# Optimization experiments

Hardware: AMD Instinct MI355X
Metric: run time of the kernel (lower is better)

Reference implementation:

```python
import jax, jax.numpy as jnp
import numpy as np

NUM_HEADS = 12
LN_EPS = 1e-5


def _pe(seq_len, d_model):
    # sinusoidal positional encoding buffer (constant)
    pos = np.arange(seq_len, dtype=np.float32)[:, None]
    div = np.exp(np.arange(0, d_model, 2, dtype=np.float32) * (-np.log(10000.0) / d_model))
    pe = np.zeros((seq_len, d_model), dtype=np.float32)
    pe[:, 0::2] = np.sin(pos * div)
    pe[:, 1::2] = np.cos(pos * div)
    return jnp.asarray(pe)


def _ln(x, g, b):
    m = jnp.mean(x, axis=-1, keepdims=True)
    v = jnp.mean(jnp.square(x - m), axis=-1, keepdims=True)
    return (x - m) * jax.lax.rsqrt(v + LN_EPS) * g + b


def setup_inputs() -> dict:
    key = jax.random.key(0)
    B, S, V, D, L, F = 8, 512, 32000, 768, 4, 3072
    ks = jax.random.split(key, 8)
    sc = 0.02
    return {
        "x_ids": jax.random.randint(ks[0], (B, S), 0, V),
        "emb": jax.random.normal(ks[1], (V, D), jnp.float32) * sc,
        "Wq": jax.random.normal(ks[2], (L, D, D), jnp.float32) * sc,
        "bq": jnp.zeros((L, D), jnp.float32),
        "Wk": jax.random.normal(ks[3], (L, D, D), jnp.float32) * sc,
        "bk": jnp.zeros((L, D), jnp.float32),
        "Wv": jax.random.normal(ks[4], (L, D, D), jnp.float32) * sc,
        "bv": jnp.zeros((L, D), jnp.float32),
        "Wo": jax.random.normal(ks[5], (L, D, D), jnp.float32) * sc,
        "bo": jnp.zeros((L, D), jnp.float32),
        "g1": jnp.ones((L, D), jnp.float32),
        "bn1": jnp.zeros((L, D), jnp.float32),
        "W1": jax.random.normal(ks[6], (L, D, F), jnp.float32) * sc,
        "bw1": jnp.zeros((L, F), jnp.float32),
        "W2": jax.random.normal(ks[7], (L, F, D), jnp.float32) * sc,
        "bw2": jnp.zeros((L, D), jnp.float32),
        "g2": jnp.ones((L, D), jnp.float32),
        "bn2": jnp.zeros((L, D), jnp.float32),
    }


def reference(x_ids, emb, Wq, bq, Wk, bk, Wv, bv, Wo, bo, g1, bn1, W1, bw1, W2, bw2, g2, bn2):
    B, S = x_ids.shape
    D = emb.shape[1]
    H = NUM_HEADS
    dk = D // H
    h = emb[x_ids] + _pe(S, D)  # [B,S,D]; dropout is identity (eval)

    def layer(h, p):
        wq, bq_, wk, bk_, wv, bv_, wo, bo_, g1_, bn1_, w1, b1_, w2, b2_, g2_, bn2_ = p

        def heads(y):  # [B,S,D] -> [B,H,S,dk]
            return y.reshape(B, S, H, dk).transpose(0, 2, 1, 3)

        q = heads(h @ wq + bq_)
        k = heads(h @ wk + bk_)
        v = heads(h @ wv + bv_)
        scores = jnp.einsum('bhqd,bhkd->bhqk', q, k) / jnp.sqrt(jnp.float32(dk))
        attn = jax.nn.softmax(scores, axis=-1)
        o = jnp.einsum('bhqk,bhkd->bhqd', attn, v)
        o = o.transpose(0, 2, 1, 3).reshape(B, S, D)
        h = _ln(h + o @ wo + bo_, g1_, bn1_)
        ff = jax.nn.relu(h @ w1 + b1_) @ w2 + b2_
        h = _ln(h + ff, g2_, bn2_)
        return h, None

    h, _ = jax.lax.scan(layer, h, (Wq, bq, Wk, bk, Wv, bv, Wo, bo, g1, bn1, W1, bw1, W2, bw2, g2, bn2))
    return h
```

## Files before the change

### kernel.cpp

```cpp
#include <hip/hip_runtime.h>
#include <stdint.h>

#define B_ 8
#define S_ 512
#define D_ 768
#define H_ 12
#define DK_ 64
#define F_ 3072
#define L_ 4
#define NT_ (B_*S_)
#define BH_ (B_*H_)
#define DQKV_ 2304

typedef __bf16 bf16x8 __attribute__((ext_vector_type(8)));
typedef float f32x4 __attribute__((ext_vector_type(4)));

static __device__ __forceinline__ unsigned short f2b(float f){
  union { float f; unsigned u; } x; x.f = f;
  unsigned r = x.u + 0x7fffu + ((x.u >> 16) & 1u);
  return (unsigned short)(r >> 16);
}
static __device__ __forceinline__ float b2f(unsigned short u){
  union { unsigned u; float f; } x; x.u = ((unsigned)u) << 16; return x.f;
}

static __device__ __forceinline__ void gload16(const void* g, void* l){
  __builtin_amdgcn_global_load_lds((const __attribute__((address_space(1))) void*)g,
                                   (__attribute__((address_space(3))) void*)l, 16, 0, 0);
}

static __device__ __forceinline__ float wsum(float v){
  #pragma unroll
  for (int off = 32; off; off >>= 1) v += __shfl_xor(v, off);
  return v;
}

__global__ void wconv_kernel(const float* __restrict__ in, unsigned short* __restrict__ out,
                             int R, int C, size_t outLS, int rowBase){
  __shared__ float tile[64][33];
  const int l = blockIdx.z;
  in  += (size_t)l*R*C;
  out += (size_t)l*outLS;
  const int c0 = blockIdx.x*32, r0 = blockIdx.y*64;
  const int tx = threadIdx.x, ty = threadIdx.y;
  #pragma unroll
  for (int i = 0; i < 8; ++i)
    tile[ty+8*i][tx] = in[(size_t)(r0+ty+8*i)*C + c0+tx];
  __syncthreads();
  #pragma unroll
  for (int p = 0; p < 4; ++p) {
    const int c = p*8 + ty;
    ushort2 u;
    u.x = f2b(tile[tx*2][c]);
    u.y = f2b(tile[tx*2+1][c]);
    *reinterpret_cast<ushort2*>(&out[(size_t)(rowBase + c0 + c)*R + r0 + tx*2]) = u;
  }
}

__global__ void wconvqkv_kernel(const float* __restrict__ Wq, const float* __restrict__ Wk,
                                const float* __restrict__ Wv, unsigned short* __restrict__ out){
  __shared__ float tile[64][33];
  const int z = blockIdx.z;
  const int l = z / 3, which = z % 3;
  const float* in = (which == 0 ? Wq : which == 1 ? Wk : Wv) + (size_t)l*D_*D_;
  unsigned short* o = out + (size_t)l*DQKV_*D_;
  const int rowBase = which*D_;
  const int c0 = blockIdx.x*32, r0 = blockIdx.y*64;
  const int tx = threadIdx.x, ty = threadIdx.y;
  #pragma unroll
  for (int i = 0; i < 8; ++i)
    tile[ty+8*i][tx] = in[(size_t)(r0+ty+8*i)*D_ + c0+tx];
  __syncthreads();
  #pragma unroll
  for (int p = 0; p < 4; ++p) {
    const int c = p*8 + ty;
    ushort2 u;
    u.x = f2b(tile[tx*2][c]);
    u.y = f2b(tile[tx*2+1][c]);
    *reinterpret_cast<ushort2*>(&o[(size_t)(rowBase + c0 + c)*D_ + r0 + tx*2]) = u;
  }
}

__global__ void bcat_kernel(const float* __restrict__ bq, const float* __restrict__ bk,
                            const float* __restrict__ bv, float* __restrict__ out){
  int i = blockIdx.x*256 + threadIdx.x;
  if (i >= L_*DQKV_) return;
  int l = i / DQKV_, c = i % DQKV_;
  float v = (c < D_) ? bq[l*D_ + c] : (c < 2*D_) ? bk[l*D_ + c - D_] : bv[l*D_ + c - 2*D_];
  out[i] = v;
}

__global__ __launch_bounds__(256) void pe_kernel(float* __restrict__ pe){
  int u = blockIdx.x*256 + threadIdx.x;
  if (u >= S_*384) return;
  int dp = u % 384, s = u / 384;
  int d0 = dp*2;
  float div = __expf((float)d0 * (-9.210340371976184f / 768.0f));
  float ang = (float)s * div;
  pe[(size_t)s*D_ + d0]     = sinf(ang);
  pe[(size_t)s*D_ + d0 + 1] = cosf(ang);
}

__global__ __launch_bounds__(256) void embed_kernel(const int* __restrict__ ids,
                                                    const float* __restrict__ emb,
                                                    const float* __restrict__ pe,
                                                    unsigned short* __restrict__ hb){
  int u = blockIdx.x*256 + threadIdx.x;
  if (u >= NT_*192) return;
  int c = u % 192, t = u / 192, s = t % S_;
  int id = ids[t];
  float4 e = reinterpret_cast<const float4*>(emb + (size_t)id*D_)[c];
  float4 p = reinterpret_cast<const float4*>(pe  + (size_t)s*D_)[c];
  ushort4 ub; ub.x = f2b(e.x+p.x); ub.y = f2b(e.y+p.y); ub.z = f2b(e.z+p.z); ub.w = f2b(e.w+p.w);
  reinterpret_cast<ushort4*>(hb + (size_t)t*D_)[c] = ub;
}

template<int TN, int KS, bool BIAS, bool RES, bool RELU>
__global__ __launch_bounds__(256)
void gemm_kernel(const unsigned short* __restrict__ A,
                 const unsigned short* __restrict__ Bt,
                 const float* __restrict__ bias,
                 const unsigned short* __restrict__ residB,
                 unsigned short* __restrict__ outp,
                 int M, int N, int K)
{
  constexpr int WN = TN/2;
  constexpr int JF = WN/16;
  constexpr int SLOTS = (128+TN)/64;
  __shared__ __attribute__((aligned(16))) unsigned short As[3][128*32];
  __shared__ __attribute__((aligned(16))) unsigned short Bs[3][TN*32];
  const int tid = threadIdx.x;
  const int w = tid >> 6, l = tid & 63;
  const int wm = w >> 1, wn = w & 1;
  const int c16 = l & 15, g = l >> 4;

  const int nwg = gridDim.x;
  const int cpx = nwg >> 3;
  const int sw  = (blockIdx.x & 7)*cpx + (blockIdx.x >> 3);
  const int nbx = N/TN;
  const int nby = M/128;
  const int bx = sw % nbx;
  const int t2 = sw / nbx;
  const int by = t2 % nby;
  const int ks = t2 / nby;
  const int bm = by*128, bn = bx*TN;
  const int Klen = K / KS;
  const int kBeg = ks*Klen;
  const int nk = Klen >> 5;

  auto stage = [&](int buf, int k0){
    #pragma unroll
    for (int s = 0; s < SLOTS; ++s) {
      const int base = s*4096 + w*1024;
      const int x    = base + l*16;
      if (s < 2) {
        const int row  = x >> 6;
        const int csrc = ((x >> 4) & 3) ^ ((row >> 2) & 3);
        gload16(A + (size_t)(bm+row)*K + k0 + csrc*8, (void*)(As[buf] + base/2));
      } else {
        const int o2   = x - 8192;
        const int row  = o2 >> 6;
        const int csrc = ((o2 >> 4) & 3) ^ ((row >> 2) & 3);
        gload16(Bt + (size_t)(bn+row)*K + k0 + csrc*8, (void*)(Bs[buf] + (base-8192)/2));
      }
    }
  };

  f32x4 acc[4][JF] = {};
  const int cswz = (g ^ (c16 >> 2)) * 8;

  stage(0, kBeg);
  stage(1, kBeg + 32);
  stage(2, kBeg + 64);

  for (int t = 0; t < nk; ++t) {
    const int cur = t % 3;
    const int rem = nk - 1 - t;
    if constexpr (SLOTS == 4) {
      if (rem >= 2)      asm volatile("s_waitcnt vmcnt(8)" ::: "memory");
      else if (rem == 1) asm volatile("s_waitcnt vmcnt(4)" ::: "memory");
      else               asm volatile("s_waitcnt vmcnt(0)" ::: "memory");
    } else {
      if (rem >= 2)      asm volatile("s_waitcnt vmcnt(6)" ::: "memory");
      else if (rem == 1) asm volatile("s_waitcnt vmcnt(3)" ::: "memory");
      else               asm volatile("s_waitcnt vmcnt(0)" ::: "memory");
    }
    __builtin_amdgcn_s_barrier();
    __builtin_amdgcn_sched_barrier(0);

    bf16x8 af[4], bfr[JF];
    #pragma unroll
    for (int i = 0; i < 4; ++i)
      af[i]  = *reinterpret_cast<const bf16x8*>(&As[cur][(wm*64 + i*16 + c16)*32 + cswz]);
    #pragma unroll
    for (int j = 0; j < JF; ++j)
      bfr[j] = *reinterpret_cast<const bf16x8*>(&Bs[cur][(wn*WN + j*16 + c16)*32 + cswz]);
    asm volatile("s_waitcnt lgkmcnt(0)" ::: "memory");
    __builtin_amdgcn_sched_barrier(0);
    __builtin_amdgcn_s_barrier();

    if (t + 3 < nk) stage(cur, kBeg + (t+3)*32);

    __builtin_amdgcn_s_setprio(1);
    #pragma unroll
    for (int i = 0; i < 4; ++i)
      #pragma unroll
      for (int j = 0; j < JF; ++j)
        acc[i][j] = __builtin_amdgcn_mfma_f32_16x16x32_bf16(af[i], bfr[j], acc[i][j], 0, 0, 0);
    __builtin_amdgcn_s_setprio(0);
  }

  unsigned short* outB = outp + (size_t)ks*M*N;
  #pragma unroll
  for (int i = 0; i < 4; ++i) {
    #pragma unroll
    for (int e = 0; e < 4; ++e) {
      const int row = bm + wm*64 + i*16 + (l>>4)*4 + e;
      #pragma unroll
      for (int j = 0; j < JF; ++j) {
        const int col = bn + wn*WN + j*16 + (l&15);
        float v = acc[i][j][e];
        if constexpr (BIAS) v += bias[col];
        if constexpr (RES)  v += b2f(residB[(size_t)row*N + col]);
        if constexpr (RELU) v = fmaxf(v, 0.f);
        outB[(size_t)row*N + col] = f2b(v);
      }
    }
  }
}

__global__ void vtrans_kernel(const unsigned short* __restrict__ v,
                              unsigned short* __restrict__ vt, int ld){
  __shared__ unsigned short tile[32][33];
  const int z = blockIdx.z; const int b = z / H_, hh = z % H_;
  const int j0 = blockIdx.x*32;
  const int d0 = blockIdx.y*32;
  const int tx = threadIdx.x, ty = threadIdx.y;
  const unsigned short* src = v + (size_t)b*S_*ld + hh*DK_;
  #pragma unroll
  for (int i = 0; i < 4; ++i)
    tile[ty+8*i][tx] = src[(size_t)(j0+ty+8*i)*ld + d0+tx];
  __syncthreads();
  unsigned short* dst = vt + (size_t)z*DK_*S_;
  #pragma unroll
  for (int i = 0; i < 4; ++i)
    dst[(size_t)(d0+ty+8*i)*S_ + j0+tx] = tile[tx][ty+8*i];
}

__global__ __launch_bounds__(256)
void fattn_kernel(const unsigned short* __restrict__ qkv,
                  const unsigned short* __restrict__ vt,
                  unsigned short* __restrict__ o)
{
  __shared__ __attribute__((aligned(16))) unsigned short Plds[4*4096];
  const int tid = threadIdx.x;
  const int w = tid >> 6, l = tid & 63;
  const int g = l >> 4, c16 = l & 15;
  const int z = blockIdx.y; const int b = z / H_, hh = z % H_;
  const int q0 = blockIdx.x*128 + w*32;

  const unsigned short* qp = qkv + (size_t)b*S_*DQKV_ + hh*DK_;
  const unsigned short* kp = qp + D_;
  const unsigned short* vv = vt + (size_t)z*DK_*S_;
  char* pbase = (char*)Plds + w*8192;

  bf16x8 qf[2][2];
  #pragma unroll
  for (int jf = 0; jf < 2; ++jf)
    #pragma unroll
    for (int kc = 0; kc < 2; ++kc)
      qf[jf][kc] = *reinterpret_cast<const bf16x8*>(qp + (size_t)(q0 + jf*16 + c16)*DQKV_ + kc*32 + g*8);

  f32x4 acc_o[2][4] = {};
  float m_run[2] = {-1e30f, -1e30f};
  float l_run[2] = {0.f, 0.f};

  for (int kb = 0; kb < S_/128; ++kb) {
    f32x4 acc_s[8][2] = {};
    #pragma unroll
    for (int kt = 0; kt < 8; ++kt) {
      bf16x8 af0 = *reinterpret_cast<const bf16x8*>(kp + (size_t)(kb*128 + kt*16 + c16)*DQKV_ + 0*32 + g*8);
      bf16x8 af1 = *reinterpret_cast<const bf16x8*>(kp + (size_t)(kb*128 + kt*16 + c16)*DQKV_ + 1*32 + g*8);
      #pragma unroll
      for (int jf = 0; jf < 2; ++jf) {
        acc_s[kt][jf] = __builtin_amdgcn_mfma_f32_16x16x32_bf16(af0, qf[jf][0], acc_s[kt][jf], 0, 0, 0);
        acc_s[kt][jf] = __builtin_amdgcn_mfma_f32_16x16x32_bf16(af1, qf[jf][1], acc_s[kt][jf], 0, 0, 0);
      }
    }
    float fac[2];
    #pragma unroll
    for (int jf = 0; jf < 2; ++jf) {
      float vmax = -1e30f;
      #pragma unroll
      for (int kt = 0; kt < 8; ++kt)
        #pragma unroll
        for (int e = 0; e < 4; ++e) {
          acc_s[kt][jf][e] *= 0.125f;
          vmax = fmaxf(vmax, acc_s[kt][jf][e]);
        }
      vmax = fmaxf(vmax, __shfl_xor(vmax, 16));
      vmax = fmaxf(vmax, __shfl_xor(vmax, 32));
      const float m_new = fmaxf(m_run[jf], vmax);
      fac[jf] = __expf(m_run[jf] - m_new);
      float ps = 0.f;
      #pragma unroll
      for (int kt = 0; kt < 8; ++kt)
        #pragma unroll
        for (int e = 0; e < 4; ++e) {
          float p = __expf(acc_s[kt][jf][e] - m_new);
          acc_s[kt][jf][e] = p;
          ps += p;
        }
      ps += __shfl_xor(ps, 16);
      ps += __shfl_xor(ps, 32);
      l_run[jf] = l_run[jf]*fac[jf] + ps;
      m_run[jf] = m_new;
      const int q = jf*16 + c16;
      #pragma unroll
      for (int kt = 0; kt < 8; ++kt) {
        uint2 val;
        val.x = (unsigned)f2b(acc_s[kt][jf][0]) | ((unsigned)f2b(acc_s[kt][jf][1]) << 16);
        val.y = (unsigned)f2b(acc_s[kt][jf][2]) | ((unsigned)f2b(acc_s[kt][jf][3]) << 16);
        int off = (q*256 + kt*32 + g*8) ^ ((q & 7) << 4);
        *reinterpret_cast<uint2*>(pbase + off) = val;
      }
    }
    #pragma unroll
    for (int jr = 0; jr < 2; ++jr)
      #pragma unroll
      for (int e = 0; e < 4; ++e) {
        const float fr = __shfl(fac[jr], g*4 + e);
        #pragma unroll
        for (int jd = 0; jd < 4; ++jd)
          acc_o[jr][jd][e] *= fr;
      }
    #pragma unroll
    for (int kc = 0; kc < 4; ++kc) {
      bf16x8 pa[2], vfr[4];
      #pragma unroll
      for (int jf = 0; jf < 2; ++jf) {
        const int q = jf*16 + c16;
        int off = (q*256 + kc*64 + g*16) ^ ((q & 7) << 4);
        pa[jf] = *reinterpret_cast<const bf16x8*>(pbase + off);
      }
      #pragma unroll
      for (int jd = 0; jd < 4; ++jd)
        vfr[jd] = *reinterpret_cast<const bf16x8*>(vv + (size_t)(jd*16 + c16)*S_ + kb*128 + kc*32 + g*8);
      #pragma unroll
      for (int jf = 0; jf < 2; ++jf)
        #pragma unroll
        for (int jd = 0; jd < 4; ++jd)
          acc_o[jf][jd] = __builtin_amdgcn_mfma_f32_16x16x32_bf16(pa[jf], vfr[jd], acc_o[jf][jd], 0, 0, 0);
    }
  }

  float invl[2] = {1.f/l_run[0], 1.f/l_run[1]};
  unsigned short* ob = o + (size_t)b*S_*D_ + hh*DK_;
  #pragma unroll
  for (int jr = 0; jr < 2; ++jr)
    #pragma unroll
    for (int e = 0; e < 4; ++e) {
      const float ir = __shfl(invl[jr], g*4 + e);
      const int r = q0 + jr*16 + g*4 + e;
      #pragma unroll
      for (int jd = 0; jd < 4; ++jd)
        ob[(size_t)r*D_ + jd*16 + c16] = f2b(acc_o[jr][jd][e] * ir);
    }
}

template<int NP, bool EXTRA, bool WF32>
__global__ __launch_bounds__(256)
void ln_kernel(const unsigned short* __restrict__ xb,
               const unsigned short* __restrict__ resid, const float* __restrict__ bias2,
               const float* __restrict__ g, const float* __restrict__ bta,
               float* __restrict__ ho, unsigned short* __restrict__ hb)
{
  const int w = threadIdx.x >> 6, l = threadIdx.x & 63;
  const size_t row = (size_t)blockIdx.x*4 + w;
  float vx[3][4]; float s1 = 0.f, s2 = 0.f;
  #pragma unroll
  for (int c = 0; c < 3; ++c) {
    ushort4 u0 = reinterpret_cast<const ushort4*>(xb + row*D_)[l + 64*c];
    vx[c][0] = b2f(u0.x); vx[c][1] = b2f(u0.y); vx[c][2] = b2f(u0.z); vx[c][3] = b2f(u0.w);
    #pragma unroll
    for (int p = 1; p < NP; ++p) {
      ushort4 up = reinterpret_cast<const ushort4*>(xb + (size_t)p*NT_*D_ + row*D_)[l + 64*c];
      vx[c][0] += b2f(up.x); vx[c][1] += b2f(up.y); vx[c][2] += b2f(up.z); vx[c][3] += b2f(up.w);
    }
    if constexpr (EXTRA) {
      ushort4 ur = reinterpret_cast<const ushort4*>(resid + row*D_)[l + 64*c];
      float4 bb = reinterpret_cast<const float4*>(bias2)[l + 64*c];
      vx[c][0] += b2f(ur.x) + bb.x; vx[c][1] += b2f(ur.y) + bb.y;
      vx[c][2] += b2f(ur.z) + bb.z; vx[c][3] += b2f(ur.w) + bb.w;
    }
    #pragma unroll
    for (int e = 0; e < 4; ++e) { s1 += vx[c][e]; s2 += vx[c][e]*vx[c][e]; }
  }
  s1 = wsum(s1); s2 = wsum(s2);
  const float mean = s1 * (1.f/768.f);
  const float var  = s2 * (1.f/768.f) - mean*mean;
  const float rs   = rsqrtf(var + 1e-5f);
  const float4* gp = reinterpret_cast<const float4*>(g);
  const float4* bp = reinterpret_cast<const float4*>(bta);
  #pragma unroll
  for (int c = 0; c < 3; ++c) {
    float4 gg = gp[l + 64*c], bb = bp[l + 64*c];
    float r0 = (vx[c][0] - mean)*rs*gg.x + bb.x;
    float r1 = (vx[c][1] - mean)*rs*gg.y + bb.y;
    float r2 = (vx[c][2] - mean)*rs*gg.z + bb.z;
    float r3 = (vx[c][3] - mean)*rs*gg.w + bb.w;
    if constexpr (WF32) {
      float4 r; r.x = r0; r.y = r1; r.z = r2; r.w = r3;
      reinterpret_cast<float4*>(ho + row*D_)[l + 64*c] = r;
    }
    ushort4 u; u.x = f2b(r0); u.y = f2b(r1); u.z = f2b(r2); u.w = f2b(r3);
    reinterpret_cast<ushort4*>(hb + row*D_)[l + 64*c] = u;
  }
}

extern "C" void kernel_launch(void* const* d_in, const int* in_sizes, int n_in,
                              void* d_out, int out_size, void* d_ws, size_t ws_size,
                              hipStream_t stream)
{
  const int*   x_ids = (const int*)  d_in[0];
  const float* emb   = (const float*)d_in[1];
  const float* Wq    = (const float*)d_in[2];
  const float* bq    = (const float*)d_in[3];
  const float* Wk    = (const float*)d_in[4];
  const float* bk    = (const float*)d_in[5];
  const float* Wv    = (const float*)d_in[6];
  const float* bv    = (const float*)d_in[7];
  const float* Wo    = (const float*)d_in[8];
  const float* bo    = (const float*)d_in[9];
  const float* g1    = (const float*)d_in[10];
  const float* bn1   = (const float*)d_in[11];
  const float* W1    = (const float*)d_in[12];
  const float* bw1   = (const float*)d_in[13];
  const float* W2    = (const float*)d_in[14];
  const float* bw2   = (const float*)d_in[15];
  const float* g2    = (const float*)d_in[16];
  const float* bn2   = (const float*)d_in[17];

  char* ws = (char*)d_ws;
  size_t off = 0;
  auto alloc = [&](size_t bytes) -> void* {
    void* p = ws + off; off += (bytes + 255) & ~((size_t)255); return p;
  };
  unsigned short* WqkvT = (unsigned short*)alloc((size_t)L_*DQKV_*D_*2);
  unsigned short* WoT = (unsigned short*)alloc((size_t)L_*D_*D_*2);
  unsigned short* W1T = (unsigned short*)alloc((size_t)L_*D_*F_*2);
  unsigned short* W2T = (unsigned short*)alloc((size_t)L_*D_*F_*2);
  float*          bqkv= (float*)         alloc((size_t)L_*DQKV_*4);
  float*          pe  = (float*)         alloc((size_t)S_*D_*4);
  unsigned short* hb  = (unsigned short*)alloc((size_t)NT_*D_*2);
  unsigned short* qkv = (unsigned short*)alloc((size_t)NT_*DQKV_*2);
  unsigned short* vt  = (unsigned short*)alloc((size_t)BH_*DK_*S_*2);
  unsigned short* attnb = (unsigned short*)alloc((size_t)NT_*D_*2);
  unsigned short* yb  = (unsigned short*)alloc((size_t)NT_*D_*2);
  unsigned short* f1b = (unsigned short*)alloc((size_t)NT_*F_*2);
  unsigned short* y2pb= (unsigned short*)alloc((size_t)4*NT_*D_*2);
  if (off > ws_size) return;

  wconvqkv_kernel<<<dim3(24,12,L_*3), dim3(32,8), 0, stream>>>(Wq, Wk, Wv, WqkvT);
  wconv_kernel<<<dim3(24,12,L_), dim3(32,8), 0, stream>>>(Wo, WoT, D_, D_, (size_t)D_*D_, 0);
  wconv_kernel<<<dim3(96,12,L_), dim3(32,8), 0, stream>>>(W1, W1T, D_, F_, (size_t)D_*F_, 0);
  wconv_kernel<<<dim3(24,48,L_), dim3(32,8), 0, stream>>>(W2, W2T, F_, D_, (size_t)F_*D_, 0);
  bcat_kernel<<<dim3((L_*DQKV_+255)/256), 256, 0, stream>>>(bq, bk, bv, bqkv);

  pe_kernel<<<dim3(S_*384/256), 256, 0, stream>>>(pe);
  embed_kernel<<<dim3(NT_*192/256), 256, 0, stream>>>(x_ids, emb, pe, hb);

  for (int l = 0; l < L_; ++l) {
    const unsigned short* wqkvT = WqkvT + (size_t)l*DQKV_*D_;
    const unsigned short* woT = WoT + (size_t)l*D_*D_;
    const unsigned short* w1T = W1T + (size_t)l*D_*F_;
    const unsigned short* w2T = W2T + (size_t)l*D_*F_;

    gemm_kernel<128,1,true,false,false><<<576, 256, 0, stream>>>(
        hb, wqkvT, bqkv + l*DQKV_, nullptr, qkv, NT_, DQKV_, D_);

    vtrans_kernel<<<dim3(16,2,BH_), dim3(32,8), 0, stream>>>(qkv + 2*D_, vt, DQKV_);
    fattn_kernel<<<dim3(S_/128, BH_), 256, 0, stream>>>(qkv, vt, attnb);

    gemm_kernel<64,1,true,true,false><<<384, 256, 0, stream>>>(
        attnb, woT, bo + l*D_, hb, yb, NT_, D_, D_);
    ln_kernel<1,false,false><<<dim3(NT_/4), 256, 0, stream>>>(yb, nullptr, nullptr,
        g1 + l*D_, bn1 + l*D_, nullptr, hb);

    gemm_kernel<128,1,true,false,true><<<768, 256, 0, stream>>>(
        hb, w1T, bw1 + l*F_, nullptr, f1b, NT_, F_, D_);
    gemm_kernel<128,4,false,false,false><<<768, 256, 0, stream>>>(
        f1b, w2T, nullptr, nullptr, y2pb, NT_, D_, F_);

    if (l == L_-1)
      ln_kernel<4,true,true><<<dim3(NT_/4), 256, 0, stream>>>(y2pb, hb, bw2 + l*D_,
          g2 + l*D_, bn2 + l*D_, (float*)d_out, hb);
    else
      ln_kernel<4,true,false><<<dim3(NT_/4), 256, 0, stream>>>(y2pb, hb, bw2 + l*D_,
          g2 + l*D_, bn2 + l*D_, nullptr, hb);
  }
}
```

Baseline: 646.3 us.

## Double-buffer LDS fragment reads in registers to overlap with MFMA

Restructures the GEMM main loop so that the LDS fragment reads for the next k-step are issued into a second register set while the MFMAs for the current step run. This removes the read-then-compute serialization and one barrier per iteration. In exchange it doubles fragment register usage, which may reduce occupancy, and it changes the vmcnt wait schedule, which needs careful correctness handling.

```diff
diff --git a/kernel.cpp b/kernel.cpp
--- a/kernel.cpp
+++ b/kernel.cpp
@@ -166,47 +166,56 @@
     }
   };
 
+  const int cswz = (g ^ (c16 >> 2)) * 8;
   f32x4 acc[4][JF] = {};
-  const int cswz = (g ^ (c16 >> 2)) * 8;
+  bf16x8 afA[4], bfA[JF], afB[4], bfB[JF];
+
+  auto frag_read = [&](bf16x8 (&af)[4], bf16x8 (&bf)[JF], int buf){
+    #pragma unroll
+    for (int i = 0; i < 4; ++i)
+      af[i] = *reinterpret_cast<const bf16x8*>(&As[buf][(wm*64 + i*16 + c16)*32 + cswz]);
+    #pragma unroll
+    for (int j = 0; j < JF; ++j)
+      bf[j] = *reinterpret_cast<const bf16x8*>(&Bs[buf][(wn*WN + j*16 + c16)*32 + cswz]);
+  };
+  auto mfma_all = [&](bf16x8 (&af)[4], bf16x8 (&bf)[JF]){
+    #pragma unroll
+    for (int i = 0; i < 4; ++i)
+      #pragma unroll
+      for (int j = 0; j < JF; ++j)
+        acc[i][j] = __builtin_amdgcn_mfma_f32_16x16x32_bf16(af[i], bf[j], acc[i][j], 0, 0, 0);
+  };
 
   stage(0, kBeg);
   stage(1, kBeg + 32);
   stage(2, kBeg + 64);
+  if constexpr (SLOTS == 4) asm volatile("s_waitcnt vmcnt(8)" ::: "memory");
+  else                      asm volatile("s_waitcnt vmcnt(6)" ::: "memory");
+  __builtin_amdgcn_s_barrier();
+  __builtin_amdgcn_sched_barrier(0);
+  frag_read(afA, bfA, 0);
 
   for (int t = 0; t < nk; ++t) {
-    const int cur = t % 3;
-    const int rem = nk - 1 - t;
-    if constexpr (SLOTS == 4) {
-      if (rem >= 2)      asm volatile("s_waitcnt vmcnt(8)" ::: "memory");
-      else if (rem == 1) asm volatile("s_waitcnt vmcnt(4)" ::: "memory");
-      else               asm volatile("s_waitcnt vmcnt(0)" ::: "memory");
-    } else {
-      if (rem >= 2)      asm volatile("s_waitcnt vmcnt(6)" ::: "memory");
-      else if (rem == 1) asm volatile("s_waitcnt vmcnt(3)" ::: "memory");
-      else               asm volatile("s_waitcnt vmcnt(0)" ::: "memory");
-    }
-    __builtin_amdgcn_s_barrier();
-    __builtin_amdgcn_sched_barrier(0);
-
-    bf16x8 af[4], bfr[JF];
-    #pragma unroll
-    for (int i = 0; i < 4; ++i)
-      af[i]  = *reinterpret_cast<const bf16x8*>(&As[cur][(wm*64 + i*16 + c16)*32 + cswz]);
-    #pragma unroll
-    for (int j = 0; j < JF; ++j)
-      bfr[j] = *reinterpret_cast<const bf16x8*>(&Bs[cur][(wn*WN + j*16 + c16)*32 + cswz]);
+    if (t <= nk-3) {
+      if constexpr (SLOTS == 4) asm volatile("s_waitcnt vmcnt(4)" ::: "memory");
+      else                      asm volatile("s_waitcnt vmcnt(3)" ::: "memory");
+    } else if (t == nk-2) {
+      asm volatile("s_waitcnt vmcnt(0)" ::: "memory");
+    }
     asm volatile("s_waitcnt lgkmcnt(0)" ::: "memory");
     __builtin_amdgcn_sched_barrier(0);
-    __builtin_amdgcn_s_barrier();
-
-    if (t + 3 < nk) stage(cur, kBeg + (t+3)*32);
-
+    if (t + 1 < nk) {
+      __builtin_amdgcn_s_barrier();
+      __builtin_amdgcn_sched_barrier(0);
+    }
+    const bool odd = t & 1;
+    if (t + 1 < nk) {
+      const int nslot = (t+1) % 3;
+      if (odd) frag_read(afA, bfA, nslot); else frag_read(afB, bfB, nslot);
+    }
+    if (t + 3 < nk) stage(t % 3, kBeg + (t+3)*32);
     __builtin_amdgcn_s_setprio(1);
-    #pragma unroll
-    for (int i = 0; i < 4; ++i)
-      #pragma unroll
-      for (int j = 0; j < JF; ++j)
-        acc[i][j] = __builtin_amdgcn_mfma_f32_16x16x32_bf16(af[i], bfr[j], acc[i][j], 0, 0, 0);
+    if (odd) mfma_all(afB, bfB); else mfma_all(afA, bfA);
     __builtin_amdgcn_s_setprio(0);
   }
 
```

Result: slower. 970.8 us (+50.2%).

## Switch GEMM mainloop to BK=64 double-buffered LDS pipeline without swizzle

Applied to the files above, without the earlier changes.

The GEMM K-tile grows from 32 to 64 and the three-stage LDS ring becomes two buffers. The next tile is prefetched between the two halves of the LDS fragment reads, and each iteration does twice the MFMAs per barrier. This halves the number of barrier and waitcnt rounds. In exchange it drops the XOR column swizzle, so the 128-byte row stride may cause LDS bank conflicts. Waiting on vmcnt(0) every iteration also leaves less load latency hidden than the deeper prefetch did.

```diff
diff --git a/kernel.cpp b/kernel.cpp
--- a/kernel.cpp
+++ b/kernel.cpp
@@ -126,9 +126,9 @@
 {
   constexpr int WN = TN/2;
   constexpr int JF = WN/16;
-  constexpr int SLOTS = (128+TN)/64;
-  __shared__ __attribute__((aligned(16))) unsigned short As[3][128*32];
-  __shared__ __attribute__((aligned(16))) unsigned short Bs[3][TN*32];
+  constexpr int BPASS = TN/32;
+  __shared__ __attribute__((aligned(16))) unsigned short As[2][128*64];
+  __shared__ __attribute__((aligned(16))) unsigned short Bs[2][TN*64];
   const int tid = threadIdx.x;
   const int w = tid >> 6, l = tid & 63;
   const int wm = w >> 1, wn = w & 1;
@@ -146,67 +146,64 @@
   const int bm = by*128, bn = bx*TN;
   const int Klen = K / KS;
   const int kBeg = ks*Klen;
-  const int nk = Klen >> 5;
+  const int nk = Klen >> 6;
 
   auto stage = [&](int buf, int k0){
     #pragma unroll
-    for (int s = 0; s < SLOTS; ++s) {
-      const int base = s*4096 + w*1024;
-      const int x    = base + l*16;
-      if (s < 2) {
-        const int row  = x >> 6;
-        const int csrc = ((x >> 4) & 3) ^ ((row >> 2) & 3);
-        gload16(A + (size_t)(bm+row)*K + k0 + csrc*8, (void*)(As[buf] + base/2));
-      } else {
-        const int o2   = x - 8192;
-        const int row  = o2 >> 6;
-        const int csrc = ((o2 >> 4) & 3) ^ ((row >> 2) & 3);
-        gload16(Bt + (size_t)(bn+row)*K + k0 + csrc*8, (void*)(Bs[buf] + (base-8192)/2));
-      }
+    for (int s = 0; s < 4; ++s) {
+      const int x = s*4096 + tid*16;
+      const int row = x >> 7, col = (x & 127) >> 1;
+      gload16(A + (size_t)(bm+row)*K + k0 + col, (void*)(As[buf] + x/2));
+    }
+    #pragma unroll
+    for (int s = 0; s < BPASS; ++s) {
+      const int x = s*4096 + tid*16;
+      const int row = x >> 7, col = (x & 127) >> 1;
+      gload16(Bt + (size_t)(bn+row)*K + k0 + col, (void*)(Bs[buf] + x/2));
     }
   };
 
   f32x4 acc[4][JF] = {};
-  const int cswz = (g ^ (c16 >> 2)) * 8;
 
   stage(0, kBeg);
-  stage(1, kBeg + 32);
-  stage(2, kBeg + 64);
 
   for (int t = 0; t < nk; ++t) {
-    const int cur = t % 3;
-    const int rem = nk - 1 - t;
-    if constexpr (SLOTS == 4) {
-      if (rem >= 2)      asm volatile("s_waitcnt vmcnt(8)" ::: "memory");
-      else if (rem == 1) asm volatile("s_waitcnt vmcnt(4)" ::: "memory");
-      else               asm volatile("s_waitcnt vmcnt(0)" ::: "memory");
-    } else {
-      if (rem >= 2)      asm volatile("s_waitcnt vmcnt(6)" ::: "memory");
-      else if (rem == 1) asm volatile("s_waitcnt vmcnt(3)" ::: "memory");
-      else               asm volatile("s_waitcnt vmcnt(0)" ::: "memory");
-    }
+    const int b = t & 1;
+    asm volatile("s_waitcnt vmcnt(0)" ::: "memory");
     __builtin_amdgcn_s_barrier();
     __builtin_amdgcn_sched_barrier(0);
 
-    bf16x8 af[4], bfr[JF];
+    bf16x8 a0[4], b0[JF], a1[4], b1[JF];
     #pragma unroll
     for (int i = 0; i < 4; ++i)
-      af[i]  = *reinterpret_cast<const bf16x8*>(&As[cur][(wm*64 + i*16 + c16)*32 + cswz]);
+      a0[i] = *reinterpret_cast<const bf16x8*>(&As[b][(wm*64 + i*16 + c16)*64 + g*8]);
     #pragma unroll
     for (int j = 0; j < JF; ++j)
-      bfr[j] = *reinterpret_cast<const bf16x8*>(&Bs[cur][(wn*WN + j*16 + c16)*32 + cswz]);
+      b0[j] = *reinterpret_cast<const bf16x8*>(&Bs[b][(wn*WN + j*16 + c16)*64 + g*8]);
+
+    if (t + 1 < nk) stage(b ^ 1, kBeg + (t+1)*64);
+
+    #pragma unroll
+    for (int i = 0; i < 4; ++i)
+      a1[i] = *reinterpret_cast<const bf16x8*>(&As[b][(wm*64 + i*16 + c16)*64 + 32 + g*8]);
+    #pragma unroll
+    for (int j = 0; j < JF; ++j)
+      b1[j] = *reinterpret_cast<const bf16x8*>(&Bs[b][(wn*WN + j*16 + c16)*64 + 32 + g*8]);
+
     asm volatile("s_waitcnt lgkmcnt(0)" ::: "memory");
     __builtin_amdgcn_sched_barrier(0);
-    __builtin_amdgcn_s_barrier();
-
-    if (t + 3 < nk) stage(cur, kBeg + (t+3)*32);
 
     __builtin_amdgcn_s_setprio(1);
     #pragma unroll
     for (int i = 0; i < 4; ++i)
       #pragma unroll
       for (int j = 0; j < JF; ++j)
-        acc[i][j] = __builtin_amdgcn_mfma_f32_16x16x32_bf16(af[i], bfr[j], acc[i][j], 0, 0, 0);
+        acc[i][j] = __builtin_amdgcn_mfma_f32_16x16x32_bf16(a0[i], b0[j], acc[i][j], 0, 0, 0);
+    #pragma unroll
+    for (int i = 0; i < 4; ++i)
+      #pragma unroll
+      for (int j = 0; j < JF; ++j)
+        acc[i][j] = __builtin_amdgcn_mfma_f32_16x16x32_bf16(a1[i], b1[j], acc[i][j], 0, 0, 0);
     __builtin_amdgcn_s_setprio(0);
   }
 
```

New measurement: 731.0 us. 1.13x slower.
